# Kernel tuning notes

Measured on AMD Instinct MI355X. Metric: run time of the kernel, lower is better.

The kernel has to match this reference:

```python
import jax, jax.numpy as jnp
import numpy as np

B, S, D = 4, 2048, 1024
N_HEAD = 16
HEAD_DIM = D // N_HEAD


def setup_inputs() -> dict:
    key = jax.random.key(0)
    k1, k2, k3 = jax.random.split(key, 3)
    std = 0.02
    return {
        "x": jax.random.normal(k1, (B, S, D), dtype=jnp.float32),
        "c_attn_w": jax.random.normal(k2, (D, 3 * D), dtype=jnp.float32) * std,
        "c_attn_b": jnp.zeros((3 * D,), dtype=jnp.float32),
        "c_proj_w": jax.random.normal(k3, (D, D), dtype=jnp.float32) * std,
        "c_proj_b": jnp.zeros((D,), dtype=jnp.float32),
    }


def _split_heads(t):
    # [B, S, D] -> [B, H, S, hd]
    b, s, d = t.shape
    return t.reshape(b, s, N_HEAD, d // N_HEAD).transpose(0, 2, 1, 3)


def reference(x, c_attn_w, c_attn_b, c_proj_w, c_proj_b):
    # fused QKV projection (TFConv1D = x @ w + b)
    qkv = x @ c_attn_w + c_attn_b                      # [B, S, 3D]
    q, k, v = jnp.split(qkv, 3, axis=2)
    q, k, v = _split_heads(q), _split_heads(k), _split_heads(v)  # [B, H, S, hd]

    # scaled scores
    w = jnp.einsum('bhqd,bhkd->bhqk', q, k)
    w = w / jnp.sqrt(jnp.asarray(HEAD_DIM, w.dtype))

    # causal mask via multiplicative trick: i >= j - ns + nd (nd == ns == S)
    nd = ns = S
    i = jnp.arange(nd)[:, None]
    j = jnp.arange(ns)[None, :]
    b = (i >= j - ns + nd).astype(w.dtype)[None, None]  # [1,1,nd,ns]
    w = w * b - 10000.0 * (1.0 - b)

    w = jax.nn.softmax(w, axis=-1)
    a = jnp.einsum('bhqk,bhkd->bhqd', w, v)            # [B, H, S, hd]

    # merge heads: [B, H, S, hd] -> [B, S, D]
    a = a.transpose(0, 2, 1, 3).reshape(x.shape[0], x.shape[1], -1)
    a = a @ c_proj_w + c_proj_b
    return a
```

## Files before the change

kernel.cpp:

```cpp
#include <hip/hip_runtime.h>
#include <hip/hip_bf16.h>

typedef unsigned short ushort_t;
typedef __attribute__((ext_vector_type(8))) short short8;
typedef __attribute__((ext_vector_type(4))) float floatx4;

#define LOG2E 1.4426950408889634f

__device__ __forceinline__ unsigned short f2bf(float f) {
    unsigned u = __float_as_uint(f);
    u += 0x7FFF + ((u >> 16) & 1);
    return (unsigned short)(u >> 16);
}

__device__ __forceinline__ void async_ld16(const void* gptr, void* lptr) {
    typedef const __attribute__((address_space(1))) unsigned int TG;
    typedef __attribute__((address_space(3))) unsigned int TL;
    __builtin_amdgcn_global_load_lds((TG*)(unsigned long long)gptr,
                                     (TL*)(unsigned)(unsigned long long)lptr,
                                     16, 0, 0);
}

__global__ __launch_bounds__(256) void prep_kernel(const float* __restrict__ x,
                                                   const float* __restrict__ wqkv,
                                                   const float* __restrict__ wproj,
                                                   ushort_t* __restrict__ xb,
                                                   ushort_t* __restrict__ wqkvT,
                                                   ushort_t* __restrict__ wprojT) {
    __shared__ float t[32][33];
    int bx = blockIdx.x;
    if (bx < 8192) {
        int i = bx * 256 + threadIdx.x;
        float4 v = ((const float4*)x)[i];
        unsigned long long r = (unsigned long long)f2bf(v.x)
                             | ((unsigned long long)f2bf(v.y) << 16)
                             | ((unsigned long long)f2bf(v.z) << 32)
                             | ((unsigned long long)f2bf(v.w) << 48);
        ((unsigned long long*)xb)[i] = r;
        return;
    }
    const float* in; ushort_t* out; int R, C, bidx;
    if (bx < 8192 + 3072) { in = wqkv; out = wqkvT; R = 1024; C = 3072; bidx = bx - 8192; }
    else                  { in = wproj; out = wprojT; R = 1024; C = 1024; bidx = bx - 11264; }
    int nbc = C >> 5;
    int bc = bidx % nbc, br = bidx / nbc;
    int tx = threadIdx.x & 31, ty = threadIdx.x >> 5;
    int r0 = br << 5, c0 = bc << 5;
#pragma unroll
    for (int j = 0; j < 4; ++j)
        t[ty + j * 8][tx] = in[(size_t)(r0 + ty + j * 8) * C + c0 + tx];
    __syncthreads();
#pragma unroll
    for (int j = 0; j < 4; ++j)
        out[(size_t)(c0 + ty + j * 8) * R + r0 + tx] = f2bf(t[tx][ty + j * 8]);
}

__global__ __launch_bounds__(512) void gemm_qkv_kernel(const ushort_t* __restrict__ A,
                                                       const ushort_t* __restrict__ Bt,
                                                       const float* __restrict__ bias,
                                                       ushort_t* __restrict__ qbuf,
                                                       ushort_t* __restrict__ kbuf,
                                                       ushort_t* __restrict__ vtbuf) {
    extern __shared__ __align__(16) ushort_t lds[];

    int bid = blockIdx.x;
    int wg = (bid & 7) * 96 + (bid >> 3);
    int bm = wg & 63, bn = wg >> 6;
    int m0 = bm << 7, n0 = bn << 8;

    int tid = threadIdx.x;
    int wave = tid >> 6, lane = tid & 63;
    int c = lane & 15, g = lane >> 4;
    int wm = wave >> 2, wn = wave & 3;

    int row0 = tid >> 3;
    int sch  = (tid & 7) ^ (row0 & 7);
    size_t aoff = (size_t)(m0 + row0) * 1024 + sch * 8;
    size_t boff = (size_t)(n0 + row0) * 1024 + sch * 8;

    int co0 = (g * 8) ^ ((c & 7) << 3);
    int co1 = co0 ^ 32;

    floatx4 acc[4][4];
    short8 a[4][2], bf[2][2], bg[2][2];
#pragma unroll
    for (int i2 = 0; i2 < 4; ++i2)
#pragma unroll
        for (int j2 = 0; j2 < 4; ++j2) { floatx4 z = {0.f,0.f,0.f,0.f}; acc[i2][j2] = z; }

    auto stA = [&](int t, int buf) {
        const ushort_t* s = A + aoff + (size_t)t * 64;
        ushort_t* d = lds + buf * 8192 + tid * 8;
        async_ld16(s, d);
        async_ld16(s + 65536, d + 4096);
    };
    auto stB = [&](int t, int h, int buf) {
        const ushort_t* s = Bt + boff + (size_t)h * 131072 + (size_t)t * 64;
        ushort_t* d = lds + 16384 + buf * 16384 + h * 8192 + tid * 8;
        async_ld16(s, d);
        async_ld16(s + 65536, d + 4096);
    };
    auto ld_a = [&](int buf) {
#pragma unroll
        for (int mi = 0; mi < 4; ++mi) {
            int ro = buf * 8192 + (wm * 64 + mi * 16 + c) * 64;
            a[mi][0] = *(const short8*)&lds[ro + co0];
            a[mi][1] = *(const short8*)&lds[ro + co1];
        }
    };
    auto ld_b = [&](int buf, int q, short8 (&bb)[2][2]) {
#pragma unroll
        for (int nii = 0; nii < 2; ++nii) {
            int ro = 16384 + buf * 16384 + (wn * 64 + (q * 2 + nii) * 16 + c) * 64;
            bb[nii][0] = *(const short8*)&lds[ro + co0];
            bb[nii][1] = *(const short8*)&lds[ro + co1];
        }
    };
    auto phase_mm = [&](int q, short8 (&bb)[2][2]) {
        asm volatile("s_barrier" ::: "memory");
        asm volatile("s_waitcnt lgkmcnt(0)" ::: "memory");
        __builtin_amdgcn_s_setprio(1);
#pragma unroll
        for (int mi = 0; mi < 4; ++mi)
#pragma unroll
            for (int nii = 0; nii < 2; ++nii)
#pragma unroll
                for (int ks = 0; ks < 2; ++ks)
                    acc[mi][q * 2 + nii] =
                        __builtin_amdgcn_mfma_f32_16x16x32_bf16(
                            a[mi][ks], bb[nii][ks], acc[mi][q * 2 + nii], 0, 0, 0);
        __builtin_amdgcn_s_setprio(0);
        asm volatile("s_barrier" ::: "memory");
    };

    stA(0, 0); stB(0, 0, 0); stB(0, 1, 0);
    stA(1, 1); stB(1, 0, 1);
    asm volatile("s_waitcnt vmcnt(4)" ::: "memory");
    asm volatile("s_barrier" ::: "memory");

#pragma unroll 1
    for (int i = 0; i < 7; ++i) {
        int t0 = 2 * i;
        ld_a(0); ld_b(0, 0, bf);
        stB(t0 + 1, 1, 1);
        stA(t0 + 2, 0);
        phase_mm(0, bf);
        ld_b(0, 1, bg);
        stB(t0 + 2, 0, 0);
        asm volatile("s_waitcnt vmcnt(4)" ::: "memory");
        phase_mm(1, bg);
        ld_a(1); ld_b(1, 0, bf);
        stB(t0 + 2, 1, 0);
        stA(t0 + 3, 1);
        phase_mm(0, bf);
        ld_b(1, 1, bg);
        stB(t0 + 3, 0, 1);
        asm volatile("s_waitcnt vmcnt(4)" ::: "memory");
        phase_mm(1, bg);
    }
    ld_a(0); ld_b(0, 0, bf);
    stB(15, 1, 1);
    phase_mm(0, bf);
    ld_b(0, 1, bg);
    asm volatile("s_waitcnt vmcnt(0)" ::: "memory");
    phase_mm(1, bg);
    ld_a(1); ld_b(1, 0, bf);
    phase_mm(0, bf);
    ld_b(1, 1, bg);
    phase_mm(1, bg);

    int sec = n0 >> 10;
    int h0 = (n0 & 1023) >> 6;
    int b  = m0 >> 11, sbase = m0 & 2047;
    int bh0 = b * 16 + h0;
    float bv[4];
#pragma unroll
    for (int ni = 0; ni < 4; ++ni) bv[ni] = bias[n0 + wn * 64 + ni * 16 + c];

    __syncthreads();

    if (sec < 2) {
        float scl = (sec == 0) ? (0.125f * LOG2E) : 1.0f;
#pragma unroll
        for (int mi = 0; mi < 4; ++mi)
#pragma unroll
            for (int ni = 0; ni < 4; ++ni)
#pragma unroll
                for (int r = 0; r < 4; ++r) {
                    int row = wm * 64 + mi * 16 + g * 4 + r;
                    lds[wn * 9216 + row * 72 + ni * 16 + c] =
                        f2bf((acc[mi][ni][r] + bv[ni]) * scl);
                }
        __syncthreads();
        ushort_t* dstbase = (sec == 0 ? qbuf : kbuf);
        int head = tid >> 7, row = tid & 127;
        const ushort_t* src = &lds[head * 9216 + row * 72];
        ushort_t* dst = dstbase + (size_t)(bh0 + head) * 131072
                      + (size_t)(sbase + row) * 64;
#pragma unroll
        for (int j = 0; j < 8; ++j)
            *(short8*)(dst + j * 8) = *(const short8*)(src + j * 8);
    } else {
#pragma unroll
        for (int mi = 0; mi < 4; ++mi)
#pragma unroll
            for (int ni = 0; ni < 4; ++ni) {
                int d = ni * 16 + c;
                int s0 = wm * 64 + mi * 16 + g * 4;
                unsigned long long pk =
                      (unsigned long long)f2bf(acc[mi][ni][0] + bv[ni])
                    | ((unsigned long long)f2bf(acc[mi][ni][1] + bv[ni]) << 16)
                    | ((unsigned long long)f2bf(acc[mi][ni][2] + bv[ni]) << 32)
                    | ((unsigned long long)f2bf(acc[mi][ni][3] + bv[ni]) << 48);
                *(unsigned long long*)&lds[wn * 8704 + d * 136 + s0] = pk;
            }
        __syncthreads();
        int head = tid >> 7, rr = (tid & 127) >> 1, half = tid & 1;
        const ushort_t* src = &lds[head * 8704 + rr * 136 + half * 64];
        ushort_t* dst = vtbuf + (size_t)(bh0 + head) * 131072
                      + (size_t)rr * 2048 + sbase + half * 64;
#pragma unroll
        for (int j = 0; j < 8; ++j)
            *(short8*)(dst + j * 8) = *(const short8*)(src + j * 8);
    }
}

__global__ __launch_bounds__(256, 6) void attn_kernel(const ushort_t* __restrict__ qb_,
                                                      const ushort_t* __restrict__ kb_,
                                                      const ushort_t* __restrict__ vtb_,
                                                      ushort_t* __restrict__ aout) {
    __shared__ __align__(16) ushort_t Ks[64 * 68];
    __shared__ __align__(16) ushort_t Vs[64 * 68];
    __shared__ __align__(16) ushort_t Ps[4][16 * 68];
    int bx = blockIdx.x;
    int qb = 31 - (bx >> 6);
    int bhix = bx & 63;
    int b = bhix >> 4, h = bhix & 15;
    int q0 = qb << 6;
    int tid = threadIdx.x, wave = tid >> 6, lane = tid & 63;
    int c = lane & 15, g = lane >> 4;
    size_t bh = (size_t)(b * 16 + h);

    const ushort_t* Qp = qb_ + (bh * 2048 + q0) * 64;
    const ushort_t* Kp = kb_ + bh * 131072;
    const ushort_t* Vp = vtb_ + bh * 131072;

    int qr = wave * 16 + c;
    short8 qf0 = *(const short8*)(Qp + qr * 64 + g * 8);
    short8 qf1 = *(const short8*)(Qp + qr * 64 + 32 + g * 8);

    float l_part = 0.f;
    floatx4 o_acc[4];
#pragma unroll
    for (int nt = 0; nt < 4; ++nt) { floatx4 z = {0.f,0.f,0.f,0.f}; o_acc[nt] = z; }

    short8 kreg[2], vreg[2];
#pragma unroll
    for (int it = 0; it < 2; ++it) {
        int idx = it * 256 + tid;
        kreg[it] = *(const short8*)(Kp + idx * 8);
        vreg[it] = *(const short8*)(Vp + (idx >> 3) * 2048 + (idx & 7) * 8);
    }

    int qg = q0 + wave * 16 + c;
    for (int kt = 0; kt <= qb; ++kt) {
        int kt0 = kt << 6;
        __syncthreads();
#pragma unroll
        for (int it = 0; it < 2; ++it) {
            int idx = it * 256 + tid;
            *(short8*)&Ks[(idx >> 3) * 68 + (idx & 7) * 8] = kreg[it];
            *(short8*)&Vs[(idx >> 3) * 68 + (idx & 7) * 8] = vreg[it];
        }
        __syncthreads();
        if (kt < qb) {
            int s0 = (kt + 1) << 6;
#pragma unroll
            for (int it = 0; it < 2; ++it) {
                int idx = it * 256 + tid;
                kreg[it] = *(const short8*)(Kp + s0 * 64 + idx * 8);
                vreg[it] = *(const short8*)(Vp + (idx >> 3) * 2048 + s0 + (idx & 7) * 8);
            }
        }
        bool diag = (kt == qb);

        float lp = 0.f;
#pragma unroll
        for (int nt = 0; nt < 4; ++nt) {
            short8 kf0 = *(const short8*)&Ks[(nt * 16 + c) * 68 + g * 8];
            short8 kf1 = *(const short8*)&Ks[(nt * 16 + c) * 68 + 32 + g * 8];
            floatx4 z = {0.f, 0.f, 0.f, 0.f};
            z = __builtin_amdgcn_mfma_f32_16x16x32_bf16(kf0, qf0, z, 0, 0, 0);
            z = __builtin_amdgcn_mfma_f32_16x16x32_bf16(kf1, qf1, z, 0, 0, 0);

            int kpb = kt0 + nt * 16 + g * 4;
            float p[4];
#pragma unroll
            for (int r = 0; r < 4; ++r) {
                float s = z[r];
                if (diag) s = (kpb + r > qg) ? -1e30f : s;
                p[r] = exp2f(s);
                lp += p[r];
            }
            union { unsigned long long u; __hip_bfloat162 h2[2]; } pk;
            pk.h2[0] = __float22bfloat162_rn(make_float2(p[0], p[1]));
            pk.h2[1] = __float22bfloat162_rn(make_float2(p[2], p[3]));
            *(unsigned long long*)&Ps[wave][c * 68 + nt * 16 + g * 4] = pk.u;
        }
        l_part += lp;

#pragma unroll
        for (int ks = 0; ks < 2; ++ks) {
            short8 pf = *(const short8*)&Ps[wave][c * 68 + ks * 32 + g * 8];
#pragma unroll
            for (int nt = 0; nt < 4; ++nt) {
                short8 vf = *(const short8*)&Vs[(nt * 16 + c) * 68 + ks * 32 + g * 8];
                o_acc[nt] = __builtin_amdgcn_mfma_f32_16x16x32_bf16(pf, vf, o_acc[nt], 0, 0, 0);
            }
        }
    }

    float l = l_part;
    l += __shfl_xor(l, 16);
    l += __shfl_xor(l, 32);
    float linv = 1.0f / l;
    float inv[4];
#pragma unroll
    for (int r = 0; r < 4; ++r)
        inv[r] = __shfl(linv, g * 4 + r);
#pragma unroll
    for (int nt = 0; nt < 4; ++nt)
#pragma unroll
        for (int r = 0; r < 4; ++r) {
            int q = q0 + wave * 16 + g * 4 + r;
            aout[(size_t)(b * 2048 + q) * 1024 + h * 64 + nt * 16 + c] =
                f2bf(o_acc[nt][r] * inv[r]);
        }
}

__global__ __launch_bounds__(256) void gemm_proj_kernel(const ushort_t* __restrict__ A,
                                                        const ushort_t* __restrict__ Bt,
                                                        const float* __restrict__ bias,
                                                        float* __restrict__ Cout) {
    const int K = 1024, N = 1024, nbn = 8;
    __shared__ __align__(16) ushort_t As[128 * 32];
    __shared__ __align__(16) ushort_t Bs[128 * 32];
    int bm = blockIdx.x / nbn, bn = blockIdx.x % nbn;
    int m0 = bm << 7, n0 = bn << 7;
    int tid = threadIdx.x;
    int wave = tid >> 6, lane = tid & 63;
    int c = lane & 15, g = lane >> 4;
    int m_off = (wave & 1) << 6, n_off = (wave >> 1) << 6;
    int ldrow = lane >> 2;
    int ldk   = (lane & 3) << 3;

    floatx4 acc[4][4];
#pragma unroll
    for (int mi = 0; mi < 4; ++mi)
#pragma unroll
        for (int ni = 0; ni < 4; ++ni) {
            floatx4 z = {0.f, 0.f, 0.f, 0.f};
            acc[mi][ni] = z;
        }

    for (int kk = 0; kk < K; kk += 32) {
        __syncthreads();
#pragma unroll
        for (int j = 0; j < 2; ++j) {
            int chunk = wave * 2 + j;
            async_ld16(A  + (size_t)(m0 + chunk * 16 + ldrow) * K + kk + ldk, &As[chunk * 512]);
            async_ld16(Bt + (size_t)(n0 + chunk * 16 + ldrow) * K + kk + ldk, &Bs[chunk * 512]);
        }
        __syncthreads();
        short8 bf[4];
#pragma unroll
        for (int ni = 0; ni < 4; ++ni)
            bf[ni] = *(const short8*)&Bs[(n_off + ni * 16 + c) * 32 + g * 8];
#pragma unroll
        for (int mi = 0; mi < 4; ++mi) {
            short8 af = *(const short8*)&As[(m_off + mi * 16 + c) * 32 + g * 8];
#pragma unroll
            for (int ni = 0; ni < 4; ++ni)
                acc[mi][ni] = __builtin_amdgcn_mfma_f32_16x16x32_bf16(af, bf[ni], acc[mi][ni], 0, 0, 0);
        }
    }

    float bv[4];
#pragma unroll
    for (int ni = 0; ni < 4; ++ni) bv[ni] = bias[n0 + n_off + ni * 16 + c];
#pragma unroll
    for (int mi = 0; mi < 4; ++mi)
#pragma unroll
        for (int ni = 0; ni < 4; ++ni)
#pragma unroll
            for (int r = 0; r < 4; ++r) {
                int row = m0 + m_off + mi * 16 + g * 4 + r;
                int col = n0 + n_off + ni * 16 + c;
                Cout[(size_t)row * N + col] = acc[mi][ni][r] + bv[ni];
            }
}

extern "C" void kernel_launch(void* const* d_in, const int* in_sizes, int n_in,
                              void* d_out, int out_size, void* d_ws, size_t ws_size,
                              hipStream_t stream) {
    const float* x        = (const float*)d_in[0];
    const float* c_attn_w = (const float*)d_in[1];
    const float* c_attn_b = (const float*)d_in[2];
    const float* c_proj_w = (const float*)d_in[3];
    const float* c_proj_b = (const float*)d_in[4];
    float* out = (float*)d_out;

    char* ws = (char*)d_ws;
    ushort_t* xb     = (ushort_t*)(ws);
    ushort_t* wqkvT  = (ushort_t*)(ws + 16777216);
    ushort_t* wprojT = (ushort_t*)(ws + 23068672);
    ushort_t* qbuf   = (ushort_t*)(ws + 25165824);
    ushort_t* kbuf   = (ushort_t*)(ws + 41943040);
    ushort_t* vtbuf  = (ushort_t*)(ws + 58720256);

    static bool s_attr_set = false;
    if (!s_attr_set) {
        (void)hipFuncSetAttribute(reinterpret_cast<const void*>(gemm_qkv_kernel),
                                  hipFuncAttributeMaxDynamicSharedMemorySize, 98304);
        s_attr_set = true;
    }

    prep_kernel<<<12288, 256, 0, stream>>>(x, c_attn_w, c_proj_w, xb, wqkvT, wprojT);
    gemm_qkv_kernel<<<768, 512, 98304, stream>>>(xb, wqkvT, c_attn_b, qbuf, kbuf, vtbuf);
    attn_kernel<<<2048, 256, 0, stream>>>(qbuf, kbuf, vtbuf, xb);
    gemm_proj_kernel<<<64 * 8, 256, 0, stream>>>(xb, wprojT, c_proj_b, out);
}
```

Measured before the change: 263.5 us.

## Use 1024-thread QKV GEMM blocks and compute softmax row sums via MFMA

The QKV GEMM goes from 512 to 1024 threads (16 waves) per block over the same 128x256 tile. Each wave now owns a 32x64 sub-tile, which halves per-thread accumulators and lets each thread issue fewer async loads. The load pipeline and the epilogue store mapping are rewritten to match. Separately, the attention kernel drops the scalar per-lane sum of probabilities and cross-lane shuffles, and instead gets row sums from an extra MFMA of P against a ones vector. That adds matrix work and sums bf16-rounded probabilities rather than fp32 ones.

```diff
diff --git a/kernel.cpp b/kernel.cpp
--- a/kernel.cpp
+++ b/kernel.cpp
@@ -55,12 +55,12 @@
         out[(size_t)(c0 + ty + j * 8) * R + r0 + tx] = f2bf(t[tx][ty + j * 8]);
 }
 
-__global__ __launch_bounds__(512) void gemm_qkv_kernel(const ushort_t* __restrict__ A,
-                                                       const ushort_t* __restrict__ Bt,
-                                                       const float* __restrict__ bias,
-                                                       ushort_t* __restrict__ qbuf,
-                                                       ushort_t* __restrict__ kbuf,
-                                                       ushort_t* __restrict__ vtbuf) {
+__global__ __launch_bounds__(1024) void gemm_qkv_kernel(const ushort_t* __restrict__ A,
+                                                        const ushort_t* __restrict__ Bt,
+                                                        const float* __restrict__ bias,
+                                                        ushort_t* __restrict__ qbuf,
+                                                        ushort_t* __restrict__ kbuf,
+                                                        ushort_t* __restrict__ vtbuf) {
     extern __shared__ __align__(16) ushort_t lds[];
 
     int bid = blockIdx.x;
@@ -81,29 +81,26 @@
     int co0 = (g * 8) ^ ((c & 7) << 3);
     int co1 = co0 ^ 32;
 
-    floatx4 acc[4][4];
-    short8 a[4][2], bf[2][2], bg[2][2];
-#pragma unroll
-    for (int i2 = 0; i2 < 4; ++i2)
+    floatx4 acc[2][4];
+    short8 a[2][2], bf[2][2], bg[2][2];
+#pragma unroll
+    for (int i2 = 0; i2 < 2; ++i2)
 #pragma unroll
         for (int j2 = 0; j2 < 4; ++j2) { floatx4 z = {0.f,0.f,0.f,0.f}; acc[i2][j2] = z; }
 
     auto stA = [&](int t, int buf) {
-        const ushort_t* s = A + aoff + (size_t)t * 64;
-        ushort_t* d = lds + buf * 8192 + tid * 8;
+        async_ld16(A + aoff + (size_t)t * 64, lds + buf * 8192 + tid * 8);
+    };
+    auto stB = [&](int t, int buf) {
+        const ushort_t* s = Bt + boff + (size_t)t * 64;
+        ushort_t* d = lds + 16384 + buf * 16384 + tid * 8;
         async_ld16(s, d);
-        async_ld16(s + 65536, d + 4096);
-    };
-    auto stB = [&](int t, int h, int buf) {
-        const ushort_t* s = Bt + boff + (size_t)h * 131072 + (size_t)t * 64;
-        ushort_t* d = lds + 16384 + buf * 16384 + h * 8192 + tid * 8;
-        async_ld16(s, d);
-        async_ld16(s + 65536, d + 4096);
+        async_ld16(s + 131072, d + 8192);
     };
     auto ld_a = [&](int buf) {
 #pragma unroll
-        for (int mi = 0; mi < 4; ++mi) {
-            int ro = buf * 8192 + (wm * 64 + mi * 16 + c) * 64;
+        for (int mi = 0; mi < 2; ++mi) {
+            int ro = buf * 8192 + (wm * 32 + mi * 16 + c) * 64;
             a[mi][0] = *(const short8*)&lds[ro + co0];
             a[mi][1] = *(const short8*)&lds[ro + co1];
         }
@@ -121,7 +118,7 @@
         asm volatile("s_waitcnt lgkmcnt(0)" ::: "memory");
         __builtin_amdgcn_s_setprio(1);
 #pragma unroll
-        for (int mi = 0; mi < 4; ++mi)
+        for (int mi = 0; mi < 2; ++mi)
 #pragma unroll
             for (int nii = 0; nii < 2; ++nii)
 #pragma unroll
@@ -133,33 +130,23 @@
         asm volatile("s_barrier" ::: "memory");
     };
 
-    stA(0, 0); stB(0, 0, 0); stB(0, 1, 0);
-    stA(1, 1); stB(1, 0, 1);
-    asm volatile("s_waitcnt vmcnt(4)" ::: "memory");
+    stA(0, 0); stB(0, 0);
+    stA(1, 1); stB(1, 1);
+    asm volatile("s_waitcnt vmcnt(3)" ::: "memory");
     asm volatile("s_barrier" ::: "memory");
 
 #pragma unroll 1
-    for (int i = 0; i < 7; ++i) {
-        int t0 = 2 * i;
-        ld_a(0); ld_b(0, 0, bf);
-        stB(t0 + 1, 1, 1);
-        stA(t0 + 2, 0);
+    for (int i = 0; i < 14; ++i) {
+        int buf = i & 1;
+        ld_a(buf); ld_b(buf, 0, bf);
+        stA(i + 2, buf);
         phase_mm(0, bf);
-        ld_b(0, 1, bg);
-        stB(t0 + 2, 0, 0);
-        asm volatile("s_waitcnt vmcnt(4)" ::: "memory");
+        ld_b(buf, 1, bg);
+        stB(i + 2, buf);
+        asm volatile("s_waitcnt vmcnt(3)" ::: "memory");
         phase_mm(1, bg);
-        ld_a(1); ld_b(1, 0, bf);
-        stB(t0 + 2, 1, 0);
-        stA(t0 + 3, 1);
-        phase_mm(0, bf);
-        ld_b(1, 1, bg);
-        stB(t0 + 3, 0, 1);
-        asm volatile("s_waitcnt vmcnt(4)" ::: "memory");
-        phase_mm(1, bg);
     }
     ld_a(0); ld_b(0, 0, bf);
-    stB(15, 1, 1);
     phase_mm(0, bf);
     ld_b(0, 1, bg);
     asm volatile("s_waitcnt vmcnt(0)" ::: "memory");
@@ -182,31 +169,31 @@
     if (sec < 2) {
         float scl = (sec == 0) ? (0.125f * LOG2E) : 1.0f;
 #pragma unroll
-        for (int mi = 0; mi < 4; ++mi)
+        for (int mi = 0; mi < 2; ++mi)
 #pragma unroll
             for (int ni = 0; ni < 4; ++ni)
 #pragma unroll
                 for (int r = 0; r < 4; ++r) {
-                    int row = wm * 64 + mi * 16 + g * 4 + r;
+                    int row = wm * 32 + mi * 16 + g * 4 + r;
                     lds[wn * 9216 + row * 72 + ni * 16 + c] =
                         f2bf((acc[mi][ni][r] + bv[ni]) * scl);
                 }
         __syncthreads();
         ushort_t* dstbase = (sec == 0 ? qbuf : kbuf);
-        int head = tid >> 7, row = tid & 127;
-        const ushort_t* src = &lds[head * 9216 + row * 72];
+        int head = tid >> 8, row = (tid >> 1) & 127, half = tid & 1;
+        const ushort_t* src = &lds[head * 9216 + row * 72 + half * 32];
         ushort_t* dst = dstbase + (size_t)(bh0 + head) * 131072
-                      + (size_t)(sbase + row) * 64;
-#pragma unroll
-        for (int j = 0; j < 8; ++j)
+                      + (size_t)(sbase + row) * 64 + half * 32;
+#pragma unroll
+        for (int j = 0; j < 4; ++j)
             *(short8*)(dst + j * 8) = *(const short8*)(src + j * 8);
     } else {
 #pragma unroll
-        for (int mi = 0; mi < 4; ++mi)
+        for (int mi = 0; mi < 2; ++mi)
 #pragma unroll
             for (int ni = 0; ni < 4; ++ni) {
                 int d = ni * 16 + c;
-                int s0 = wm * 64 + mi * 16 + g * 4;
+                int s0 = wm * 32 + mi * 16 + g * 4;
                 unsigned long long pk =
                       (unsigned long long)f2bf(acc[mi][ni][0] + bv[ni])
                     | ((unsigned long long)f2bf(acc[mi][ni][1] + bv[ni]) << 16)
@@ -215,12 +202,12 @@
                 *(unsigned long long*)&lds[wn * 8704 + d * 136 + s0] = pk;
             }
         __syncthreads();
-        int head = tid >> 7, rr = (tid & 127) >> 1, half = tid & 1;
-        const ushort_t* src = &lds[head * 8704 + rr * 136 + half * 64];
+        int head = tid >> 8, dd = (tid >> 2) & 63, sq = tid & 3;
+        const ushort_t* src = &lds[head * 8704 + dd * 136 + sq * 32];
         ushort_t* dst = vtbuf + (size_t)(bh0 + head) * 131072
-                      + (size_t)rr * 2048 + sbase + half * 64;
-#pragma unroll
-        for (int j = 0; j < 8; ++j)
+                      + (size_t)dd * 2048 + sbase + sq * 32;
+#pragma unroll
+        for (int j = 0; j < 4; ++j)
             *(short8*)(dst + j * 8) = *(const short8*)(src + j * 8);
     }
 }
@@ -249,8 +236,12 @@
     short8 qf0 = *(const short8*)(Qp + qr * 64 + g * 8);
     short8 qf1 = *(const short8*)(Qp + qr * 64 + 32 + g * 8);
 
-    float l_part = 0.f;
+    short8 vones;
+#pragma unroll
+    for (int j = 0; j < 8; ++j) vones[j] = (short)0x3F80;
+
     floatx4 o_acc[4];
+    floatx4 lacc = {0.f, 0.f, 0.f, 0.f};
 #pragma unroll
     for (int nt = 0; nt < 4; ++nt) { floatx4 z = {0.f,0.f,0.f,0.f}; o_acc[nt] = z; }
 
@@ -284,7 +275,6 @@
         }
         bool diag = (kt == qb);
 
-        float lp = 0.f;
 #pragma unroll
         for (int nt = 0; nt < 4; ++nt) {
             short8 kf0 = *(const short8*)&Ks[(nt * 16 + c) * 68 + g * 8];
@@ -300,18 +290,17 @@
                 float s = z[r];
                 if (diag) s = (kpb + r > qg) ? -1e30f : s;
                 p[r] = exp2f(s);
-                lp += p[r];
             }
             union { unsigned long long u; __hip_bfloat162 h2[2]; } pk;
             pk.h2[0] = __float22bfloat162_rn(make_float2(p[0], p[1]));
             pk.h2[1] = __float22bfloat162_rn(make_float2(p[2], p[3]));
             *(unsigned long long*)&Ps[wave][c * 68 + nt * 16 + g * 4] = pk.u;
         }
-        l_part += lp;
 
 #pragma unroll
         for (int ks = 0; ks < 2; ++ks) {
             short8 pf = *(const short8*)&Ps[wave][c * 68 + ks * 32 + g * 8];
+            lacc = __builtin_amdgcn_mfma_f32_16x16x32_bf16(pf, vones, lacc, 0, 0, 0);
 #pragma unroll
             for (int nt = 0; nt < 4; ++nt) {
                 short8 vf = *(const short8*)&Vs[(nt * 16 + c) * 68 + ks * 32 + g * 8];
@@ -320,14 +309,10 @@
         }
     }
 
-    float l = l_part;
-    l += __shfl_xor(l, 16);
-    l += __shfl_xor(l, 32);
-    float linv = 1.0f / l;
     float inv[4];
 #pragma unroll
     for (int r = 0; r < 4; ++r)
-        inv[r] = __shfl(linv, g * 4 + r);
+        inv[r] = 1.0f / lacc[r];
 #pragma unroll
     for (int nt = 0; nt < 4; ++nt)
 #pragma unroll
@@ -426,7 +411,7 @@
     }
 
     prep_kernel<<<12288, 256, 0, stream>>>(x, c_attn_w, c_proj_w, xb, wqkvT, wprojT);
-    gemm_qkv_kernel<<<768, 512, 98304, stream>>>(xb, wqkvT, c_attn_b, qbuf, kbuf, vtbuf);
+    gemm_qkv_kernel<<<768, 1024, 98304, stream>>>(xb, wqkvT, c_attn_b, qbuf, kbuf, vtbuf);
     attn_kernel<<<2048, 256, 0, stream>>>(qbuf, kbuf, vtbuf, xb);
     gemm_proj_kernel<<<64 * 8, 256, 0, stream>>>(xb, wprojT, c_proj_b, out);
 }
```

Result: slower. 279.2 us (+6.0%).
